# Performance work log

Hardware: AMD Instinct MI355X
Metric: run time of the kernel (lower is better)

## Reference

```python
import jax, jax.numpy as jnp
import numpy as np

EPS = 1e-10
COMMITMENT_COST = 0.25


def setup_inputs() -> dict:
    key = jax.random.key(0)
    k1, k2, k3, k4 = jax.random.split(key, 4)
    return {
        "x": jax.random.normal(k1, (32, 64, 64, 64), dtype=jnp.float32),  # NCHW, C=D=64
        "emb0": jax.random.normal(k2, (512, 64), dtype=jnp.float32),
        "emb1": jax.random.normal(k3, (512, 64), dtype=jnp.float32),
        "emb2": jax.random.normal(k4, (512, 64), dtype=jnp.float32),
        "idx": 1,
    }


def reference(x, emb0, emb1, emb2, idx):
    # NCHW -> NHWC, flatten to [N, D]
    inputs = jnp.transpose(x, (0, 2, 3, 1))
    in_shape = inputs.shape
    D = in_shape[-1]
    flat = inputs.reshape(-1, D)  # [N, D]

    if idx == 0:
        codes = emb0
    elif idx == 1:
        codes = jnp.concatenate([emb0, emb1], axis=0)
    else:
        codes = jnp.concatenate([emb0, emb2], axis=0)  # [K, D]

    distances = (
        jnp.sum(flat * flat, axis=1, keepdims=True)
        + jnp.sum(codes * codes, axis=1)
        - 2.0 * jnp.matmul(flat, codes.T)
    )
    enc_idx = jnp.argmin(distances, axis=1)  # [N]

    # one-hot @ codes is just a gather
    quantized = codes[enc_idx].reshape(in_shape)

    e_latent_loss = jnp.mean((jax.lax.stop_gradient(quantized) - inputs) ** 2)
    q_latent_loss = jnp.mean((quantized - jax.lax.stop_gradient(inputs)) ** 2)
    loss = q_latent_loss + COMMITMENT_COST * e_latent_loss

    # straight-through estimator
    quantized_st = inputs + jax.lax.stop_gradient(quantized - inputs)

    K = codes.shape[0]
    N = flat.shape[0]
    avg_probs = jnp.zeros((K,), dtype=flat.dtype).at[enc_idx].add(1.0) / N
    perplexity = jnp.exp(-jnp.sum(avg_probs * jnp.log(avg_probs + EPS)))

    return jnp.transpose(quantized_st, (0, 3, 1, 2)), loss, perplexity
```

## Files before the change

kernel.cpp:

```cpp
#include <hip/hip_runtime.h>
#include <math.h>

#define NROWS   131072
#define DFEAT   64
#define KHALF   512
#define HW      4096
#define CHW     262144
#define NQOUT   8388608
#define NBLK    1024

typedef __attribute__((ext_vector_type(8))) short   bf16x8;
typedef __attribute__((ext_vector_type(4))) float   f32x4;

__device__ __forceinline__ unsigned short f2bf(float f) {
    unsigned int u = __float_as_uint(f);
    u += 0x7FFFu + ((u >> 16) & 1u);
    return (unsigned short)(u >> 16);
}
__device__ __forceinline__ float bf2f(unsigned short h) {
    return __uint_as_float(((unsigned int)h) << 16);
}

__global__ void vq_prep(const float* __restrict__ e0, const float* __restrict__ e1,
                        const float* __restrict__ e2, const int* __restrict__ idxp,
                        float* __restrict__ wsf, float* __restrict__ cnh,
                        unsigned short* __restrict__ fragbuf) {
    int tau = blockIdx.x * 256 + threadIdx.x;
    if (tau < 1536) wsf[tau] = 0.f;

    int idx = idxp[0];
    const float* sel = (idx == 2) ? e2 : e1;

    if (tau < 1024) {
        const float* row = (tau < KHALF) ? (e0 + (size_t)tau * DFEAT)
                                         : (sel + (size_t)(tau - KHALF) * DFEAT);
        float s = 0.f;
#pragma unroll
        for (int c = 0; c < DFEAT; ++c) s = fmaf(row[c], row[c], s);
        cnh[tau] = 0.5f * s;
    }

    int tile = tau >> 8;
    int rem  = tau & 255;
    int f    = rem >> 6;
    int L    = rem & 63;
    int code = tile * 16 + (L & 15);
    int kb   = (f & 1) * 32 + (L >> 4) * 8;
    int lo_f = f >> 1;
    const float* src = (code < KHALF) ? (e0 + (size_t)code * DFEAT)
                                      : (sel + (size_t)(code - KHALF) * DFEAT);
    unsigned short* dst = fragbuf + (size_t)tau * 8;
#pragma unroll
    for (int j = 0; j < 8; ++j) {
        float v = src[kb + j];
        unsigned short hb = f2bf(v);
        dst[j] = lo_f ? f2bf(v - bf2f(hb)) : hb;
    }
}

#define TILE_STEP(BC0, BC1, BC2, BC3, CNC, BN0, BN1, BN2, BN3, CNN, TT, TL)   \
    {                                                                          \
        const int tl_ = (TL);                                                  \
        BN0 = fb[(tl_ * 4 + 0) * 64 + L];                                      \
        BN1 = fb[(tl_ * 4 + 1) * 64 + L];                                      \
        BN2 = fb[(tl_ * 4 + 2) * 64 + L];                                      \
        BN3 = fb[(tl_ * 4 + 3) * 64 + L];                                      \
        CNN = cnh[tl_ * 16 + m];                                               \
        const int kt_ = (TT) * 16 + m;                                         \
        _Pragma("unroll")                                                      \
        for (int rt = 0; rt < 2; ++rt) {                                       \
            f32x4 acc = {0.f, 0.f, 0.f, 0.f};                                  \
            acc = __builtin_amdgcn_mfma_f32_16x16x32_bf16(ahi[rt][0], BC0, acc, 0, 0, 0); \
            acc = __builtin_amdgcn_mfma_f32_16x16x32_bf16(ahi[rt][1], BC1, acc, 0, 0, 0); \
            acc = __builtin_amdgcn_mfma_f32_16x16x32_bf16(ahi[rt][0], BC2, acc, 0, 0, 0); \
            acc = __builtin_amdgcn_mfma_f32_16x16x32_bf16(ahi[rt][1], BC3, acc, 0, 0, 0); \
            acc = __builtin_amdgcn_mfma_f32_16x16x32_bf16(alo[rt][0], BC0, acc, 0, 0, 0); \
            acc = __builtin_amdgcn_mfma_f32_16x16x32_bf16(alo[rt][1], BC1, acc, 0, 0, 0); \
            acc = __builtin_amdgcn_mfma_f32_16x16x32_bf16(alo[rt][0], BC2, acc, 0, 0, 0); \
            acc = __builtin_amdgcn_mfma_f32_16x16x32_bf16(alo[rt][1], BC3, acc, 0, 0, 0); \
            _Pragma("unroll")                                                  \
            for (int r = 0; r < 4; ++r) {                                      \
                float s = acc[r] - CNC;                                        \
                if (s > best[rt * 4 + r]) { best[rt * 4 + r] = s; bidx[rt * 4 + r] = kt_; } \
            }                                                                  \
        }                                                                      \
    }

__global__ __launch_bounds__(256, 4) void vq_main(
        const float* __restrict__ x,
        const float* __restrict__ e0, const float* __restrict__ e1,
        const float* __restrict__ e2, const int* __restrict__ idxp,
        const float* __restrict__ cnh, const unsigned short* __restrict__ fragbuf,
        float* __restrict__ out, float* __restrict__ loss_acc,
        int* __restrict__ hist) {
    __shared__ float xsq_s[128];
    __shared__ float sc_s[128];
    __shared__ int   bk_s[128];

    const int t = threadIdx.x;
    const int w = t >> 6;
    const int L = t & 63;
    const int q = L >> 4;
    const int m = L & 15;

    const int rowbase = blockIdx.x * 128;
    const int n  = rowbase >> 12;
    const int s0 = rowbase & 4095;

    const int idx = idxp[0];
    const float* sel = (idx == 2) ? e2 : e1;
    const int ntiles = (idx == 0) ? 32 : 64;

    bf16x8 ahi[2][2], alo[2][2];
    const float* xb = x + (size_t)n * CHW + (s0 + w * 32);
#pragma unroll
    for (int rt = 0; rt < 2; ++rt) {
        const float* xr = xb + rt * 16 + m;
        float xs = 0.f;
#pragma unroll
        for (int h = 0; h < 2; ++h) {
#pragma unroll
            for (int j = 0; j < 8; ++j) {
                int c = h * 32 + q * 8 + j;
                float v = xr[(size_t)c * HW];
                xs = fmaf(v, v, xs);
                unsigned short hb = f2bf(v);
                unsigned short lb = f2bf(v - bf2f(hb));
                ahi[rt][h][j] = (short)hb;
                alo[rt][h][j] = (short)lb;
            }
        }
        xs += __shfl_xor(xs, 16, 64);
        xs += __shfl_xor(xs, 32, 64);
        if (q == 0) xsq_s[w * 32 + rt * 16 + m] = xs;
    }

    const bf16x8* fb = (const bf16x8*)fragbuf;
    float best[8];
    int   bidx[8];
#pragma unroll
    for (int i = 0; i < 8; ++i) { best[i] = -3.4e38f; bidx[i] = 0; }

    bf16x8 X0 = fb[0 * 64 + L];
    bf16x8 X1 = fb[1 * 64 + L];
    bf16x8 X2 = fb[2 * 64 + L];
    bf16x8 X3 = fb[3 * 64 + L];
    float  Xc = cnh[m];
    bf16x8 Y0, Y1, Y2, Y3;
    float  Yc;

    for (int tt = 0; tt < ntiles; tt += 2) {
        TILE_STEP(X0, X1, X2, X3, Xc, Y0, Y1, Y2, Y3, Yc, tt, tt + 1);
        const int t2 = (tt + 2 < ntiles) ? tt + 2 : ntiles - 1;
        TILE_STEP(Y0, Y1, Y2, Y3, Yc, X0, X1, X2, X3, Xc, tt + 1, t2);
    }

#pragma unroll
    for (int i = 0; i < 8; ++i) {
        float b = best[i]; int k = bidx[i];
#pragma unroll
        for (int off = 1; off < 16; off <<= 1) {
            float ob = __shfl_xor(b, off, 64);
            int   ok = __shfl_xor(k, off, 64);
            if (ob > b || (ob == b && ok < k)) { b = ob; k = ok; }
        }
        if (m == 0) {
            int row = w * 32 + (i >> 2) * 16 + q * 4 + (i & 3);
            sc_s[row] = b; bk_s[row] = k;
        }
    }
    __syncthreads();

    if (t < 128) {
        const int k = bk_s[t];
        float dist = xsq_s[t] - 2.f * sc_s[t];
        float l = dist;
#pragma unroll
        for (int off = 32; off > 0; off >>= 1) l += __shfl_down(l, off, 64);
        if (L == 0) atomicAdd(loss_acc, l);
        atomicAdd(&hist[k], 1);
    }

    {
        const int row  = t & 127;
        const int half = t >> 7;
        const int k = bk_s[row];
        const float* cp = ((k < KHALF) ? (e0 + (size_t)k * DFEAT)
                                       : (sel + (size_t)(k - KHALF) * DFEAT)) + half * 32;
        const float4* cp4 = (const float4*)cp;
        float* op = out + (size_t)n * CHW + (s0 + row);
#pragma unroll
        for (int c4 = 0; c4 < 8; ++c4) {
            float4 v = cp4[c4];
            int c = half * 32 + 4 * c4;
            op[(size_t)(c + 0) * HW] = v.x;
            op[(size_t)(c + 1) * HW] = v.y;
            op[(size_t)(c + 2) * HW] = v.z;
            op[(size_t)(c + 3) * HW] = v.w;
        }
    }
}

__global__ void vq_finalize(const float* __restrict__ wsf, const int* __restrict__ hist,
                            float* __restrict__ out) {
    __shared__ double partial[16];
    const int t = threadIdx.x;
    double p = (double)hist[t] / (double)NROWS;
    double term = p * log(p + 1e-10);
#pragma unroll
    for (int off = 32; off > 0; off >>= 1) term += __shfl_down(term, off, 64);
    if ((t & 63) == 0) partial[t >> 6] = term;
    __syncthreads();
    if (t == 0) {
        double s = 0.0;
        for (int i = 0; i < 16; ++i) s += partial[i];
        out[NQOUT + 1] = (float)exp(-s);
        out[NQOUT]     = 1.25f * (wsf[0] / (float)NQOUT);
    }
}

extern "C" void kernel_launch(void* const* d_in, const int* in_sizes, int n_in,
                              void* d_out, int out_size, void* d_ws, size_t ws_size,
                              hipStream_t stream) {
    const float* x  = (const float*)d_in[0];
    const float* e0 = (const float*)d_in[1];
    const float* e1 = (const float*)d_in[2];
    const float* e2 = (const float*)d_in[3];
    const int* idxp = (const int*)d_in[4];
    float* out = (float*)d_out;

    float* wsf      = (float*)d_ws;
    float* loss_acc = wsf;
    int*   hist     = (int*)(wsf + 256);
    float* cnh      = wsf + 2048;
    unsigned short* fragbuf = (unsigned short*)(wsf + 4096);

    vq_prep<<<64, 256, 0, stream>>>(e0, e1, e2, idxp, wsf, cnh, fragbuf);
    vq_main<<<NBLK, 256, 0, stream>>>(x, e0, e1, e2, idxp, cnh, fragbuf,
                                      out, loss_acc, hist);
    vq_finalize<<<1, 1024, 0, stream>>>(wsf, hist, out);
}
```

Baseline: 172.0 us.

## Halve rows per block, fold code-norm bias into MFMA accumulator init, raise occupancy

Each wave now handles 16 rows instead of 32, so the grid doubles to 2048 blocks of 64 rows. Register use for the A fragments and the best/index arrays halves, and launch bounds ask for 6 blocks per CU instead of 4. The negated code norm now seeds the MFMA accumulator, which removes a subtraction per element. The cost is that each codebook fragment loaded from global memory is reused across half as many rows, which doubles codebook traffic per output row.

```diff
diff --git a/kernel.cpp b/kernel.cpp
--- a/kernel.cpp
+++ b/kernel.cpp
@@ -7,7 +7,7 @@
 #define HW      4096
 #define CHW     262144
 #define NQOUT   8388608
-#define NBLK    1024
+#define NBLK    2048
 
 typedef __attribute__((ext_vector_type(8))) short   bf16x8;
 typedef __attribute__((ext_vector_type(4))) float   f32x4;
@@ -65,37 +65,33 @@
         BN1 = fb[(tl_ * 4 + 1) * 64 + L];                                      \
         BN2 = fb[(tl_ * 4 + 2) * 64 + L];                                      \
         BN3 = fb[(tl_ * 4 + 3) * 64 + L];                                      \
-        CNN = cnh[tl_ * 16 + m];                                               \
+        CNN = -cnh[tl_ * 16 + m];                                              \
         const int kt_ = (TT) * 16 + m;                                         \
+        f32x4 acc = {CNC, CNC, CNC, CNC};                                      \
+        acc = __builtin_amdgcn_mfma_f32_16x16x32_bf16(ahi0, BC0, acc, 0, 0, 0); \
+        acc = __builtin_amdgcn_mfma_f32_16x16x32_bf16(ahi1, BC1, acc, 0, 0, 0); \
+        acc = __builtin_amdgcn_mfma_f32_16x16x32_bf16(ahi0, BC2, acc, 0, 0, 0); \
+        acc = __builtin_amdgcn_mfma_f32_16x16x32_bf16(ahi1, BC3, acc, 0, 0, 0); \
+        acc = __builtin_amdgcn_mfma_f32_16x16x32_bf16(alo0, BC0, acc, 0, 0, 0); \
+        acc = __builtin_amdgcn_mfma_f32_16x16x32_bf16(alo1, BC1, acc, 0, 0, 0); \
+        acc = __builtin_amdgcn_mfma_f32_16x16x32_bf16(alo0, BC2, acc, 0, 0, 0); \
+        acc = __builtin_amdgcn_mfma_f32_16x16x32_bf16(alo1, BC3, acc, 0, 0, 0); \
         _Pragma("unroll")                                                      \
-        for (int rt = 0; rt < 2; ++rt) {                                       \
-            f32x4 acc = {0.f, 0.f, 0.f, 0.f};                                  \
-            acc = __builtin_amdgcn_mfma_f32_16x16x32_bf16(ahi[rt][0], BC0, acc, 0, 0, 0); \
-            acc = __builtin_amdgcn_mfma_f32_16x16x32_bf16(ahi[rt][1], BC1, acc, 0, 0, 0); \
-            acc = __builtin_amdgcn_mfma_f32_16x16x32_bf16(ahi[rt][0], BC2, acc, 0, 0, 0); \
-            acc = __builtin_amdgcn_mfma_f32_16x16x32_bf16(ahi[rt][1], BC3, acc, 0, 0, 0); \
-            acc = __builtin_amdgcn_mfma_f32_16x16x32_bf16(alo[rt][0], BC0, acc, 0, 0, 0); \
-            acc = __builtin_amdgcn_mfma_f32_16x16x32_bf16(alo[rt][1], BC1, acc, 0, 0, 0); \
-            acc = __builtin_amdgcn_mfma_f32_16x16x32_bf16(alo[rt][0], BC2, acc, 0, 0, 0); \
-            acc = __builtin_amdgcn_mfma_f32_16x16x32_bf16(alo[rt][1], BC3, acc, 0, 0, 0); \
-            _Pragma("unroll")                                                  \
-            for (int r = 0; r < 4; ++r) {                                      \
-                float s = acc[r] - CNC;                                        \
-                if (s > best[rt * 4 + r]) { best[rt * 4 + r] = s; bidx[rt * 4 + r] = kt_; } \
-            }                                                                  \
+        for (int r = 0; r < 4; ++r) {                                          \
+            if (acc[r] > best[r]) { best[r] = acc[r]; bidx[r] = kt_; }         \
         }                                                                      \
     }
 
-__global__ __launch_bounds__(256, 4) void vq_main(
+__global__ __launch_bounds__(256, 6) void vq_main(
         const float* __restrict__ x,
         const float* __restrict__ e0, const float* __restrict__ e1,
         const float* __restrict__ e2, const int* __restrict__ idxp,
         const float* __restrict__ cnh, const unsigned short* __restrict__ fragbuf,
         float* __restrict__ out, float* __restrict__ loss_acc,
         int* __restrict__ hist) {
-    __shared__ float xsq_s[128];
-    __shared__ float sc_s[128];
-    __shared__ int   bk_s[128];
+    __shared__ float xsq_s[64];
+    __shared__ float sc_s[64];
+    __shared__ int   bk_s[64];
 
     const int t = threadIdx.x;
     const int w = t >> 6;
@@ -103,7 +99,7 @@
     const int q = L >> 4;
     const int m = L & 15;
 
-    const int rowbase = blockIdx.x * 128;
+    const int rowbase = blockIdx.x * 64;
     const int n  = rowbase >> 12;
     const int s0 = rowbase & 4095;
 
@@ -111,14 +107,13 @@
     const float* sel = (idx == 2) ? e2 : e1;
     const int ntiles = (idx == 0) ? 32 : 64;
 
-    bf16x8 ahi[2][2], alo[2][2];
-    const float* xb = x + (size_t)n * CHW + (s0 + w * 32);
-#pragma unroll
-    for (int rt = 0; rt < 2; ++rt) {
-        const float* xr = xb + rt * 16 + m;
+    bf16x8 ahi0, ahi1, alo0, alo1;
+    {
+        const float* xr = x + (size_t)n * CHW + (s0 + w * 16) + m;
         float xs = 0.f;
 #pragma unroll
         for (int h = 0; h < 2; ++h) {
+            bf16x8 hi, lo;
 #pragma unroll
             for (int j = 0; j < 8; ++j) {
                 int c = h * 32 + q * 8 + j;
@@ -126,26 +121,27 @@
                 xs = fmaf(v, v, xs);
                 unsigned short hb = f2bf(v);
                 unsigned short lb = f2bf(v - bf2f(hb));
-                ahi[rt][h][j] = (short)hb;
-                alo[rt][h][j] = (short)lb;
+                hi[j] = (short)hb;
+                lo[j] = (short)lb;
             }
+            if (h == 0) { ahi0 = hi; alo0 = lo; } else { ahi1 = hi; alo1 = lo; }
         }
         xs += __shfl_xor(xs, 16, 64);
         xs += __shfl_xor(xs, 32, 64);
-        if (q == 0) xsq_s[w * 32 + rt * 16 + m] = xs;
+        if (q == 0) xsq_s[w * 16 + m] = xs;
     }
 
     const bf16x8* fb = (const bf16x8*)fragbuf;
-    float best[8];
-    int   bidx[8];
-#pragma unroll
-    for (int i = 0; i < 8; ++i) { best[i] = -3.4e38f; bidx[i] = 0; }
+    float best[4];
+    int   bidx[4];
+#pragma unroll
+    for (int i = 0; i < 4; ++i) { best[i] = -3.4e38f; bidx[i] = 0; }
 
     bf16x8 X0 = fb[0 * 64 + L];
     bf16x8 X1 = fb[1 * 64 + L];
     bf16x8 X2 = fb[2 * 64 + L];
     bf16x8 X3 = fb[3 * 64 + L];
-    float  Xc = cnh[m];
+    float  Xc = -cnh[m];
     bf16x8 Y0, Y1, Y2, Y3;
     float  Yc;
 
@@ -156,7 +152,7 @@
     }
 
 #pragma unroll
-    for (int i = 0; i < 8; ++i) {
+    for (int i = 0; i < 4; ++i) {
         float b = best[i]; int k = bidx[i];
 #pragma unroll
         for (int off = 1; off < 16; off <<= 1) {
@@ -165,13 +161,13 @@
             if (ob > b || (ob == b && ok < k)) { b = ob; k = ok; }
         }
         if (m == 0) {
-            int row = w * 32 + (i >> 2) * 16 + q * 4 + (i & 3);
+            int row = w * 16 + q * 4 + i;
             sc_s[row] = b; bk_s[row] = k;
         }
     }
     __syncthreads();
 
-    if (t < 128) {
+    if (t < 64) {
         const int k = bk_s[t];
         float dist = xsq_s[t] - 2.f * sc_s[t];
         float l = dist;
@@ -182,17 +178,17 @@
     }
 
     {
-        const int row  = t & 127;
-        const int half = t >> 7;
+        const int row  = t & 63;
+        const int quad = t >> 6;
         const int k = bk_s[row];
         const float* cp = ((k < KHALF) ? (e0 + (size_t)k * DFEAT)
-                                       : (sel + (size_t)(k - KHALF) * DFEAT)) + half * 32;
+                                       : (sel + (size_t)(k - KHALF) * DFEAT)) + quad * 16;
         const float4* cp4 = (const float4*)cp;
         float* op = out + (size_t)n * CHW + (s0 + row);
 #pragma unroll
-        for (int c4 = 0; c4 < 8; ++c4) {
+        for (int c4 = 0; c4 < 4; ++c4) {
             float4 v = cp4[c4];
-            int c = half * 32 + 4 * c4;
+            int c = quad * 16 + 4 * c4;
             op[(size_t)(c + 0) * HW] = v.x;
             op[(size_t)(c + 1) * HW] = v.y;
             op[(size_t)(c + 2) * HW] = v.z;
```

After: 192.2 us. +11.7%, slower.

## Stage codebook fragments through LDS cooperatively and fold code norm into accumulator

Applied to the files above, without the earlier changes.

Each wave used to load all four codebook fragments per tile straight from global memory. Now each wave loads one fragment into a double-buffered LDS stage shared by the block, and all waves read the four fragments from LDS, with a block barrier per tile. This cuts redundant global/L2 traffic fourfold. The negated code norm now seeds the MFMA accumulator, which removes a subtraction per element. The cost is two __syncthreads per tile pair and extra LDS use, which may reduce overlap across waves.

```diff
diff --git a/kernel.cpp b/kernel.cpp
--- a/kernel.cpp
+++ b/kernel.cpp
@@ -58,30 +58,23 @@
     }
 }
 
-#define TILE_STEP(BC0, BC1, BC2, BC3, CNC, BN0, BN1, BN2, BN3, CNN, TT, TL)   \
+#define MFMA_TILE(B0, B1, B2, B3, CN, KT)                                      \
     {                                                                          \
-        const int tl_ = (TL);                                                  \
-        BN0 = fb[(tl_ * 4 + 0) * 64 + L];                                      \
-        BN1 = fb[(tl_ * 4 + 1) * 64 + L];                                      \
-        BN2 = fb[(tl_ * 4 + 2) * 64 + L];                                      \
-        BN3 = fb[(tl_ * 4 + 3) * 64 + L];                                      \
-        CNN = cnh[tl_ * 16 + m];                                               \
-        const int kt_ = (TT) * 16 + m;                                         \
+        const int kt_ = (KT);                                                  \
         _Pragma("unroll")                                                      \
         for (int rt = 0; rt < 2; ++rt) {                                       \
-            f32x4 acc = {0.f, 0.f, 0.f, 0.f};                                  \
-            acc = __builtin_amdgcn_mfma_f32_16x16x32_bf16(ahi[rt][0], BC0, acc, 0, 0, 0); \
-            acc = __builtin_amdgcn_mfma_f32_16x16x32_bf16(ahi[rt][1], BC1, acc, 0, 0, 0); \
-            acc = __builtin_amdgcn_mfma_f32_16x16x32_bf16(ahi[rt][0], BC2, acc, 0, 0, 0); \
-            acc = __builtin_amdgcn_mfma_f32_16x16x32_bf16(ahi[rt][1], BC3, acc, 0, 0, 0); \
-            acc = __builtin_amdgcn_mfma_f32_16x16x32_bf16(alo[rt][0], BC0, acc, 0, 0, 0); \
-            acc = __builtin_amdgcn_mfma_f32_16x16x32_bf16(alo[rt][1], BC1, acc, 0, 0, 0); \
-            acc = __builtin_amdgcn_mfma_f32_16x16x32_bf16(alo[rt][0], BC2, acc, 0, 0, 0); \
-            acc = __builtin_amdgcn_mfma_f32_16x16x32_bf16(alo[rt][1], BC3, acc, 0, 0, 0); \
+            f32x4 acc = {CN, CN, CN, CN};                                      \
+            acc = __builtin_amdgcn_mfma_f32_16x16x32_bf16(ahi[rt][0], B0, acc, 0, 0, 0); \
+            acc = __builtin_amdgcn_mfma_f32_16x16x32_bf16(ahi[rt][1], B1, acc, 0, 0, 0); \
+            acc = __builtin_amdgcn_mfma_f32_16x16x32_bf16(ahi[rt][0], B2, acc, 0, 0, 0); \
+            acc = __builtin_amdgcn_mfma_f32_16x16x32_bf16(ahi[rt][1], B3, acc, 0, 0, 0); \
+            acc = __builtin_amdgcn_mfma_f32_16x16x32_bf16(alo[rt][0], B0, acc, 0, 0, 0); \
+            acc = __builtin_amdgcn_mfma_f32_16x16x32_bf16(alo[rt][1], B1, acc, 0, 0, 0); \
+            acc = __builtin_amdgcn_mfma_f32_16x16x32_bf16(alo[rt][0], B2, acc, 0, 0, 0); \
+            acc = __builtin_amdgcn_mfma_f32_16x16x32_bf16(alo[rt][1], B3, acc, 0, 0, 0); \
             _Pragma("unroll")                                                  \
             for (int r = 0; r < 4; ++r) {                                      \
-                float s = acc[r] - CNC;                                        \
-                if (s > best[rt * 4 + r]) { best[rt * 4 + r] = s; bidx[rt * 4 + r] = kt_; } \
+                if (acc[r] > best[rt * 4 + r]) { best[rt * 4 + r] = acc[r]; bidx[rt * 4 + r] = kt_; } \
             }                                                                  \
         }                                                                      \
     }
@@ -93,9 +86,10 @@
         const float* __restrict__ cnh, const unsigned short* __restrict__ fragbuf,
         float* __restrict__ out, float* __restrict__ loss_acc,
         int* __restrict__ hist) {
-    __shared__ float xsq_s[128];
-    __shared__ float sc_s[128];
-    __shared__ int   bk_s[128];
+    __shared__ float  xsq_s[128];
+    __shared__ float  sc_s[128];
+    __shared__ int    bk_s[128];
+    __shared__ bf16x8 ldsf[2][4][64];
 
     const int t = threadIdx.x;
     const int w = t >> 6;
@@ -141,18 +135,39 @@
 #pragma unroll
     for (int i = 0; i < 8; ++i) { best[i] = -3.4e38f; bidx[i] = 0; }
 
-    bf16x8 X0 = fb[0 * 64 + L];
-    bf16x8 X1 = fb[1 * 64 + L];
-    bf16x8 X2 = fb[2 * 64 + L];
-    bf16x8 X3 = fb[3 * 64 + L];
-    float  Xc = cnh[m];
-    bf16x8 Y0, Y1, Y2, Y3;
-    float  Yc;
+    bf16x8 P = fb[(0 * 4 + w) * 64 + L];
+    ldsf[0][w][L] = P;
+    P = fb[(1 * 4 + w) * 64 + L];
+    __syncthreads();
+    float Xc = -cnh[m];
+    float Yc;
+    bf16x8 Q;
 
     for (int tt = 0; tt < ntiles; tt += 2) {
-        TILE_STEP(X0, X1, X2, X3, Xc, Y0, Y1, Y2, Y3, Yc, tt, tt + 1);
-        const int t2 = (tt + 2 < ntiles) ? tt + 2 : ntiles - 1;
-        TILE_STEP(Y0, Y1, Y2, Y3, Yc, X0, X1, X2, X3, Xc, tt + 1, t2);
+        {
+            const int tq = (tt + 2 < ntiles) ? tt + 2 : ntiles - 1;
+            Q  = fb[(tq * 4 + w) * 64 + L];
+            Yc = -cnh[(tt + 1) * 16 + m];
+            bf16x8 b0 = ldsf[0][0][L];
+            bf16x8 b1 = ldsf[0][1][L];
+            bf16x8 b2 = ldsf[0][2][L];
+            bf16x8 b3 = ldsf[0][3][L];
+            MFMA_TILE(b0, b1, b2, b3, Xc, tt * 16 + m);
+            ldsf[1][w][L] = P;
+            __syncthreads();
+        }
+        {
+            const int tp = (tt + 3 < ntiles) ? tt + 3 : ntiles - 1;
+            P  = fb[(tp * 4 + w) * 64 + L];
+            Xc = -cnh[((tt + 2 < ntiles) ? tt + 2 : ntiles - 1) * 16 + m];
+            bf16x8 b0 = ldsf[1][0][L];
+            bf16x8 b1 = ldsf[1][1][L];
+            bf16x8 b2 = ldsf[1][2][L];
+            bf16x8 b3 = ldsf[1][3][L];
+            MFMA_TILE(b0, b1, b2, b3, Yc, (tt + 1) * 16 + m);
+            ldsf[0][w][L] = Q;
+            __syncthreads();
+        }
     }
 
 #pragma unroll
```

Result: no change. 170.0 us (-1.2%).
